# Kernel tuning notes

Measured on AMD Instinct MI355X. Metric: run time of the kernel, lower is better.

## Reference

```python
import jax, jax.numpy as jnp
import numpy as np

B, V, K, D, E, NE = 32, 512, 16, 128, 32, 8192


def setup_inputs() -> dict:
    key = jax.random.key(0)
    ks = jax.random.split(key, 12)
    s = 0.05
    return {
        "vertex_features": jax.random.normal(ks[0], (B, V, D), jnp.float32),
        "atom_adj": jax.random.randint(ks[1], (B * V * K,), 0, B * V),
        "bond_adj": jax.random.randint(ks[2], (B * V * K,), 0, B * NE),
        "h0": jax.random.normal(ks[3], (B, V, D), jnp.float32),
        "lamda": jnp.full((1,), 0.5, jnp.float32),
        "alpha": jnp.full((1,), 0.1, jnp.float32),
        "l": 1,
        "edge_initial": jax.random.normal(ks[4], (B, NE, E), jnp.float32),
        "vertex_mask": jnp.ones((B, V), jnp.float32),
        "nbs_mask": jax.random.uniform(ks[5], (B, V, K), jnp.float32),
        # label_U1: (D+E) -> D ; label_U2: 2D -> D ; feature_updating: D -> D (variant=False)
        "W1": jax.random.normal(ks[6], (D, D + E), jnp.float32) * s,
        "b1": jax.random.normal(ks[7], (D,), jnp.float32) * s,
        "W2": jax.random.normal(ks[8], (D, 2 * D), jnp.float32) * s,
        "b2": jax.random.normal(ks[9], (D,), jnp.float32) * s,
        "W3": jax.random.normal(ks[10], (D, D), jnp.float32) * s,
        "b3": jax.random.normal(ks[11], (D,), jnp.float32) * s,
    }


def reference(vertex_features, atom_adj, bond_adj, h0, lamda, alpha, l,
              edge_initial, vertex_mask, nbs_mask, W1, b1, W2, b2, W3, b3):
    b, v = vertex_mask.shape
    k = nbs_mask.shape[2]
    d = vertex_features.shape[-1]
    e = edge_initial.shape[-1]
    # gather neighbor vertex and edge features (flat index, torch.index_select semantics)
    vn = vertex_features.reshape(-1, d)[atom_adj].reshape(b, v, k, d)
    en = edge_initial.reshape(-1, e)[bond_adj].reshape(b, v, k, e)
    l_neighbor = jnp.concatenate([vn, en], axis=-1)            # [b,v,k,d+e]
    nl = jax.nn.gelu(l_neighbor @ W1.T + b1, approximate=False)  # exact GELU like torch F.gelu
    nl = jnp.sum(nl * nbs_mask[..., None], axis=-2)            # masked sum over neighbors -> [b,v,d]
    hi = jnp.concatenate([nl, vertex_features], axis=-1) @ W2.T + b2
    theta = jnp.log(lamda / l + 1.0)                           # broadcast scalar (shape [1])
    support = (1.0 - alpha) * hi + alpha * h0                  # variant=False: r == support
    out = theta * (support @ W3.T + b3) + (1.0 - theta) * support
    out = out + vertex_features                                # residual=True
    return out
```

## Files before the change

### kernel.cpp

```cpp
#include <hip/hip_runtime.h>
#include <hip/hip_bf16.h>
#include <math.h>

#define NLSTR 136

typedef __bf16 bf16x8 __attribute__((ext_vector_type(8)));
typedef float f32x4 __attribute__((ext_vector_type(4)));
typedef float f32x16 __attribute__((ext_vector_type(16)));
typedef unsigned short ushort8v __attribute__((ext_vector_type(8)));

union FragU { ushort8v u; bf16x8 b; };

static __device__ inline unsigned short f2bf(float f){
  unsigned u = __float_as_uint(f);
  u += 0x7fffu + ((u >> 16) & 1u);
  return (unsigned short)(u >> 16);
}
static __device__ inline float bf2f(unsigned short u){
  return __uint_as_float(((unsigned)u) << 16);
}

static __device__ inline float gelu_f(float x){
  float u = x * x;
  float p = fmaf(u, 0.07135481283f, 1.5957691216f);
  float t = x * p;
  float e = __builtin_amdgcn_exp2f(t * -1.44269504f);
  return x * __builtin_amdgcn_rcpf(1.0f + e);
}

__global__ __launch_bounds__(256) void prep_kernel(
    const float* __restrict__ vf, const float* __restrict__ W1,
    const float* __restrict__ W2, const float* __restrict__ W3,
    unsigned short* __restrict__ vfbf, unsigned short* __restrict__ w1f,
    unsigned short* __restrict__ w2f, unsigned short* __restrict__ w3f)
{
  int t = blockIdx.x * 256 + threadIdx.x;
  if (t < 262144){
    const float4* src = (const float4*)vf;
    float4 x = src[t * 2], y = src[t * 2 + 1];
    ushort8v o;
    o[0]=f2bf(x.x); o[1]=f2bf(x.y); o[2]=f2bf(x.z); o[3]=f2bf(x.w);
    o[4]=f2bf(y.x); o[5]=f2bf(y.y); o[6]=f2bf(y.z); o[7]=f2bf(y.w);
    *(ushort8v*)(vfbf + t * 8) = o;
    return;
  }
  int t2 = t - 262144;
  const float* s;
  unsigned short* d;
  if (t2 < 2560){
    int fragid = t2 >> 6, lane = t2 & 63;
    int kc = fragid >> 2, nc2 = fragid & 3, n = lane & 31, h = lane >> 5;
    s = W1 + (nc2 * 32 + n) * 160 + kc * 16 + h * 8;
    d = w1f + t2 * 8;
  } else if (t2 < 6656){
    int t3 = t2 - 2560;
    int fragid = t3 >> 6, lane = t3 & 63;
    int kc = fragid >> 3, nc = fragid & 7, col = lane & 15, quad = lane >> 4;
    s = W2 + (nc * 16 + col) * 256 + kc * 32 + quad * 8;
    d = w2f + t3 * 8;
  } else if (t2 < 8704){
    int t3 = t2 - 6656;
    int fragid = t3 >> 6, lane = t3 & 63;
    int kc = fragid >> 3, nc = fragid & 7, col = lane & 15, quad = lane >> 4;
    s = W3 + (nc * 16 + col) * 128 + kc * 32 + quad * 8;
    d = w3f + t3 * 8;
  } else return;
#pragma unroll
  for (int j = 0; j < 8; j++) d[j] = f2bf(s[j]);
}

__global__ __launch_bounds__(256) void fused_kernel(
    const unsigned short* __restrict__ vfbf,
    const int* __restrict__ aadj, const int* __restrict__ badj,
    const float* __restrict__ edge, const float* __restrict__ nbs,
    const float* __restrict__ h0,
    const unsigned short* __restrict__ w1f, const unsigned short* __restrict__ w2f,
    const unsigned short* __restrict__ w3f,
    const float* __restrict__ b1, const float* __restrict__ b2, const float* __restrict__ b3,
    const float* __restrict__ lamda, const float* __restrict__ alpha,
    const int* __restrict__ lval,
    float* __restrict__ out)
{
  __shared__ __align__(16) unsigned short nl_lds[16 * NLSTR];
  __shared__ __align__(16) unsigned short sup_lds[16 * NLSTR];
  const int wid  = threadIdx.x >> 6;
  const int lane = threadIdx.x & 63;
  const int n32  = lane & 31;
  const int h    = lane >> 5;
  const int nb   = lane & 15;
  const int vsel = (lane >> 4) & 1;
  const int col  = lane & 15;
  const int quad = lane >> 4;
  const int v0   = blockIdx.x * 16;

  float b1v[4];
#pragma unroll
  for (int nc2 = 0; nc2 < 4; nc2++) b1v[nc2] = b1[nc2 * 32 + n32];

  const ushort8v* w1v = (const ushort8v*)w1f;
  const float4*   nbs4 = (const float4*)nbs;

  for (int itp = 0; itp < 2; ++itp){
    const int vA  = v0 + wid * 4 + itp * 2;
    const int vtx = vA + vsel;
    const int a = aadj[vtx * 16 + nb];
    const int e = badj[vtx * 16 + nb];

    ushort8v av[8];
    const ushort8v* arow = (const ushort8v*)(vfbf + (size_t)a * 128 + h * 8);
#pragma unroll
    for (int kc = 0; kc < 8; kc++) av[kc] = arow[kc * 2];
    float4 e0a = *(const float4*)(edge + (size_t)e * 32 + h * 8);
    float4 e0b = *(const float4*)(edge + (size_t)e * 32 + h * 8 + 4);
    float4 e1a = *(const float4*)(edge + (size_t)e * 32 + 16 + h * 8);
    float4 e1b = *(const float4*)(edge + (size_t)e * 32 + 16 + h * 8 + 4);
    const float4 mAlo = nbs4[vA * 4 + h],       mAhi = nbs4[vA * 4 + 2 + h];
    const float4 mBlo = nbs4[(vA + 1) * 4 + h], mBhi = nbs4[(vA + 1) * 4 + 2 + h];

    FragU ef[2];
    ef[0].u[0]=f2bf(e0a.x); ef[0].u[1]=f2bf(e0a.y); ef[0].u[2]=f2bf(e0a.z); ef[0].u[3]=f2bf(e0a.w);
    ef[0].u[4]=f2bf(e0b.x); ef[0].u[5]=f2bf(e0b.y); ef[0].u[6]=f2bf(e0b.z); ef[0].u[7]=f2bf(e0b.w);
    ef[1].u[0]=f2bf(e1a.x); ef[1].u[1]=f2bf(e1a.y); ef[1].u[2]=f2bf(e1a.z); ef[1].u[3]=f2bf(e1a.w);
    ef[1].u[4]=f2bf(e1b.x); ef[1].u[5]=f2bf(e1b.y); ef[1].u[6]=f2bf(e1b.z); ef[1].u[7]=f2bf(e1b.w);

    f32x16 acc[4] = {};
#pragma unroll
    for (int kc = 0; kc < 10; kc++){
      FragU fa;
      if (kc < 8) fa.u = av[kc];
      else        fa.u = ef[kc - 8].u;
#pragma unroll
      for (int nc2 = 0; nc2 < 4; nc2++){
        FragU bf_;
        bf_.u = w1v[(kc * 4 + nc2) * 64 + lane];
        acc[nc2] = __builtin_amdgcn_mfma_f32_32x32x16_bf16(fa.b, bf_.b, acc[nc2], 0, 0, 0);
      }
    }

    const int row = wid * 4 + itp * 2;
#pragma unroll
    for (int nc2 = 0; nc2 < 4; nc2++){
      const float bb = b1v[nc2];
      f32x16 ac = acc[nc2];
      float sA = gelu_f(ac[0] + bb) * mAlo.x + gelu_f(ac[1] + bb) * mAlo.y
               + gelu_f(ac[2] + bb) * mAlo.z + gelu_f(ac[3] + bb) * mAlo.w
               + gelu_f(ac[4] + bb) * mAhi.x + gelu_f(ac[5] + bb) * mAhi.y
               + gelu_f(ac[6] + bb) * mAhi.z + gelu_f(ac[7] + bb) * mAhi.w;
      float sB = gelu_f(ac[8] + bb) * mBlo.x + gelu_f(ac[9] + bb) * mBlo.y
               + gelu_f(ac[10] + bb) * mBlo.z + gelu_f(ac[11] + bb) * mBlo.w
               + gelu_f(ac[12] + bb) * mBhi.x + gelu_f(ac[13] + bb) * mBhi.y
               + gelu_f(ac[14] + bb) * mBhi.z + gelu_f(ac[15] + bb) * mBhi.w;
      sA += __shfl_xor(sA, 32, 64);
      sB += __shfl_xor(sB, 32, 64);
      if (h == 0) nl_lds[row * NLSTR + nc2 * 32 + n32] = f2bf(sA);
      else        nl_lds[(row + 1) * NLSTR + nc2 * 32 + n32] = f2bf(sB);
    }
  }
  __syncthreads();

  const int nc0 = 2 * wid;
  const float th = logf(lamda[0] / (float)lval[0] + 1.0f);
  const float al = alpha[0];

  f32x4 acc2[2] = {};
#pragma unroll
  for (int kc = 0; kc < 8; kc++){
    FragU a;
    if (kc < 4) a.u = *(const ushort8v*)(nl_lds + col * NLSTR + kc * 32 + quad * 8);
    else        a.u = *(const ushort8v*)(vfbf + (size_t)(v0 + col) * 128 + (kc - 4) * 32 + quad * 8);
#pragma unroll
    for (int p = 0; p < 2; p++){
      FragU bf_;
      bf_.u = *(const ushort8v*)(w2f + ((kc * 8 + nc0 + p) * 64 + lane) * 8);
      acc2[p] = __builtin_amdgcn_mfma_f32_16x16x32_bf16(a.b, bf_.b, acc2[p], 0, 0, 0);
    }
  }

  float sup[2][4];
#pragma unroll
  for (int p = 0; p < 2; p++){
    const int d = (nc0 + p) * 16 + col;
    const float bb = b2[d];
#pragma unroll
    for (int r = 0; r < 4; r++){
      const int vtx = v0 + quad * 4 + r;
      float hi = acc2[p][r] + bb;
      float s = (1.f - al) * hi + al * h0[vtx * 128 + d];
      sup[p][r] = s;
      sup_lds[(quad * 4 + r) * NLSTR + d] = f2bf(s);
    }
  }
  __syncthreads();

  f32x4 acc3[2] = {};
#pragma unroll
  for (int kc = 0; kc < 4; kc++){
    FragU a;
    a.u = *(const ushort8v*)(sup_lds + col * NLSTR + kc * 32 + quad * 8);
#pragma unroll
    for (int p = 0; p < 2; p++){
      FragU bf_;
      bf_.u = *(const ushort8v*)(w3f + ((kc * 8 + nc0 + p) * 64 + lane) * 8);
      acc3[p] = __builtin_amdgcn_mfma_f32_16x16x32_bf16(a.b, bf_.b, acc3[p], 0, 0, 0);
    }
  }

#pragma unroll
  for (int p = 0; p < 2; p++){
    const int d = (nc0 + p) * 16 + col;
    const float bb = b3[d];
#pragma unroll
    for (int r = 0; r < 4; r++){
      const int vtx = v0 + quad * 4 + r;
      float res = bf2f(vfbf[(size_t)vtx * 128 + d]);
      out[vtx * 128 + d] = th * (acc3[p][r] + bb) + (1.f - th) * sup[p][r] + res;
    }
  }
}

extern "C" void kernel_launch(void* const* d_in, const int* in_sizes, int n_in,
                              void* d_out, int out_size, void* d_ws, size_t ws_size,
                              hipStream_t stream)
{
  const float* vfp  = (const float*)d_in[0];
  const int*   aadj = (const int*)d_in[1];
  const int*   badj = (const int*)d_in[2];
  const float* h0   = (const float*)d_in[3];
  const float* lam  = (const float*)d_in[4];
  const float* alp  = (const float*)d_in[5];
  const int*   lv   = (const int*)d_in[6];
  const float* edge = (const float*)d_in[7];
  const float* nbs  = (const float*)d_in[9];
  const float* W1   = (const float*)d_in[10];
  const float* b1   = (const float*)d_in[11];
  const float* W2   = (const float*)d_in[12];
  const float* b2   = (const float*)d_in[13];
  const float* W3   = (const float*)d_in[14];
  const float* b3   = (const float*)d_in[15];
  float* out = (float*)d_out;

  unsigned short* w1f  = (unsigned short*)d_ws;
  unsigned short* w2f  = w1f + 20480;
  unsigned short* w3f  = w2f + 32768;
  unsigned short* vfbf = w3f + 16384;

  prep_kernel<<<1058, 256, 0, stream>>>(vfp, W1, W2, W3, vfbf, w1f, w2f, w3f);
  fused_kernel<<<1024, 256, 0, stream>>>(vfbf, aadj, badj, edge, nbs, h0,
                                         w1f, w2f, w3f, b1, b2, b3, lam, alp, lv, out);
}
```

Measured before the change: 149.8 us.

## Stage W1 in LDS, software-pipeline neighbor gathers, use packed bf16 converts

Each block now copies the pre-swizzled W1 fragments (40KB) into shared memory and reads the MFMA B operands from LDS instead of global memory. The two-iteration neighbor loop is unrolled by hand so the second gather (vertex rows, edge features, masks) is issued before the first iteration's GELU/mask reduction, overlapping gather latency with compute. Scalar fp32-to-bf16 rounding is replaced with the packed float2-to-bfloat162 conversion. The extra 40KB of LDS per block and the higher register pressure may reduce occupancy.

```diff
diff --git a/kernel.cpp b/kernel.cpp
--- a/kernel.cpp
+++ b/kernel.cpp
@@ -18,6 +18,17 @@
 }
 static __device__ inline float bf2f(unsigned short u){
   return __uint_as_float(((unsigned)u) << 16);
+}
+static __device__ inline unsigned pk2(float a, float b){
+  union { __hip_bfloat162 h; unsigned u; } r;
+  r.h = __float22bfloat162_rn(float2{a, b});
+  return r.u;
+}
+static __device__ inline ushort8v pkcvt8(float4 a, float4 b){
+  union { unsigned u[4]; ushort8v v; } r;
+  r.u[0] = pk2(a.x, a.y); r.u[1] = pk2(a.z, a.w);
+  r.u[2] = pk2(b.x, b.y); r.u[3] = pk2(b.z, b.w);
+  return r.v;
 }
 
 static __device__ inline float gelu_f(float x){
@@ -38,10 +49,7 @@
   if (t < 262144){
     const float4* src = (const float4*)vf;
     float4 x = src[t * 2], y = src[t * 2 + 1];
-    ushort8v o;
-    o[0]=f2bf(x.x); o[1]=f2bf(x.y); o[2]=f2bf(x.z); o[3]=f2bf(x.w);
-    o[4]=f2bf(y.x); o[5]=f2bf(y.y); o[6]=f2bf(y.z); o[7]=f2bf(y.w);
-    *(ushort8v*)(vfbf + t * 8) = o;
+    *(ushort8v*)(vfbf + t * 8) = pkcvt8(x, y);
     return;
   }
   int t2 = t - 262144;
@@ -81,6 +89,7 @@
     const int* __restrict__ lval,
     float* __restrict__ out)
 {
+  __shared__ __align__(16) ushort8v w1s[2560];
   __shared__ __align__(16) unsigned short nl_lds[16 * NLSTR];
   __shared__ __align__(16) unsigned short sup_lds[16 * NLSTR];
   const int wid  = threadIdx.x >> 6;
@@ -93,63 +102,133 @@
   const int quad = lane >> 4;
   const int v0   = blockIdx.x * 16;
 
+  {
+    const ushort8v* src = (const ushort8v*)w1f;
+#pragma unroll
+    for (int i = 0; i < 10; i++)
+      w1s[threadIdx.x + 256 * i] = src[threadIdx.x + 256 * i];
+  }
+
   float b1v[4];
 #pragma unroll
   for (int nc2 = 0; nc2 < 4; nc2++) b1v[nc2] = b1[nc2 * 32 + n32];
 
-  const ushort8v* w1v = (const ushort8v*)w1f;
-  const float4*   nbs4 = (const float4*)nbs;
-
-  for (int itp = 0; itp < 2; ++itp){
-    const int vA  = v0 + wid * 4 + itp * 2;
-    const int vtx = vA + vsel;
-    const int a = aadj[vtx * 16 + nb];
-    const int e = badj[vtx * 16 + nb];
-
-    ushort8v av[8];
-    const ushort8v* arow = (const ushort8v*)(vfbf + (size_t)a * 128 + h * 8);
-#pragma unroll
-    for (int kc = 0; kc < 8; kc++) av[kc] = arow[kc * 2];
-    float4 e0a = *(const float4*)(edge + (size_t)e * 32 + h * 8);
-    float4 e0b = *(const float4*)(edge + (size_t)e * 32 + h * 8 + 4);
-    float4 e1a = *(const float4*)(edge + (size_t)e * 32 + 16 + h * 8);
-    float4 e1b = *(const float4*)(edge + (size_t)e * 32 + 16 + h * 8 + 4);
-    const float4 mAlo = nbs4[vA * 4 + h],       mAhi = nbs4[vA * 4 + 2 + h];
-    const float4 mBlo = nbs4[(vA + 1) * 4 + h], mBhi = nbs4[(vA + 1) * 4 + 2 + h];
-
-    FragU ef[2];
-    ef[0].u[0]=f2bf(e0a.x); ef[0].u[1]=f2bf(e0a.y); ef[0].u[2]=f2bf(e0a.z); ef[0].u[3]=f2bf(e0a.w);
-    ef[0].u[4]=f2bf(e0b.x); ef[0].u[5]=f2bf(e0b.y); ef[0].u[6]=f2bf(e0b.z); ef[0].u[7]=f2bf(e0b.w);
-    ef[1].u[0]=f2bf(e1a.x); ef[1].u[1]=f2bf(e1a.y); ef[1].u[2]=f2bf(e1a.z); ef[1].u[3]=f2bf(e1a.w);
-    ef[1].u[4]=f2bf(e1b.x); ef[1].u[5]=f2bf(e1b.y); ef[1].u[6]=f2bf(e1b.z); ef[1].u[7]=f2bf(e1b.w);
-
-    f32x16 acc[4] = {};
-#pragma unroll
-    for (int kc = 0; kc < 10; kc++){
-      FragU fa;
-      if (kc < 8) fa.u = av[kc];
-      else        fa.u = ef[kc - 8].u;
-#pragma unroll
-      for (int nc2 = 0; nc2 < 4; nc2++){
-        FragU bf_;
-        bf_.u = w1v[(kc * 4 + nc2) * 64 + lane];
-        acc[nc2] = __builtin_amdgcn_mfma_f32_32x32x16_bf16(fa.b, bf_.b, acc[nc2], 0, 0, 0);
-      }
-    }
-
-    const int row = wid * 4 + itp * 2;
+  const float4* nbs4 = (const float4*)nbs;
+  const int vA0 = v0 + wid * 4;
+
+  const int a0 = aadj[(vA0 + vsel) * 16 + nb];
+  const int e0 = badj[(vA0 + vsel) * 16 + nb];
+  ushort8v av0[8];
+  {
+    const ushort8v* arow = (const ushort8v*)(vfbf + (size_t)a0 * 128 + h * 8);
+#pragma unroll
+    for (int kc = 0; kc < 8; kc++) av0[kc] = arow[kc * 2];
+  }
+  float4 e0a = *(const float4*)(edge + (size_t)e0 * 32 + h * 8);
+  float4 e0b = *(const float4*)(edge + (size_t)e0 * 32 + h * 8 + 4);
+  float4 e0c = *(const float4*)(edge + (size_t)e0 * 32 + 16 + h * 8);
+  float4 e0d = *(const float4*)(edge + (size_t)e0 * 32 + 16 + h * 8 + 4);
+  const float4 m0Alo = nbs4[vA0 * 4 + h],       m0Ahi = nbs4[vA0 * 4 + 2 + h];
+  const float4 m0Blo = nbs4[(vA0 + 1) * 4 + h], m0Bhi = nbs4[(vA0 + 1) * 4 + 2 + h];
+
+  __syncthreads();
+
+  FragU ef0[2];
+  ef0[0].u = pkcvt8(e0a, e0b);
+  ef0[1].u = pkcvt8(e0c, e0d);
+
+  f32x16 acc[4] = {};
+#pragma unroll
+  for (int kc = 0; kc < 8; kc++){
+    FragU fa; fa.u = av0[kc];
+#pragma unroll
+    for (int nc2 = 0; nc2 < 4; nc2++){
+      FragU bf_; bf_.u = w1s[(kc * 4 + nc2) * 64 + lane];
+      acc[nc2] = __builtin_amdgcn_mfma_f32_32x32x16_bf16(fa.b, bf_.b, acc[nc2], 0, 0, 0);
+    }
+  }
+#pragma unroll
+  for (int kc = 8; kc < 10; kc++){
+    FragU fa; fa.u = ef0[kc - 8].u;
+#pragma unroll
+    for (int nc2 = 0; nc2 < 4; nc2++){
+      FragU bf_; bf_.u = w1s[(kc * 4 + nc2) * 64 + lane];
+      acc[nc2] = __builtin_amdgcn_mfma_f32_32x32x16_bf16(fa.b, bf_.b, acc[nc2], 0, 0, 0);
+    }
+  }
+
+  const int a1 = aadj[(vA0 + 2 + vsel) * 16 + nb];
+  const int e1 = badj[(vA0 + 2 + vsel) * 16 + nb];
+  ushort8v av1[8];
+  {
+    const ushort8v* arow = (const ushort8v*)(vfbf + (size_t)a1 * 128 + h * 8);
+#pragma unroll
+    for (int kc = 0; kc < 8; kc++) av1[kc] = arow[kc * 2];
+  }
+  float4 e1a = *(const float4*)(edge + (size_t)e1 * 32 + h * 8);
+  float4 e1b = *(const float4*)(edge + (size_t)e1 * 32 + h * 8 + 4);
+  float4 e1c = *(const float4*)(edge + (size_t)e1 * 32 + 16 + h * 8);
+  float4 e1d = *(const float4*)(edge + (size_t)e1 * 32 + 16 + h * 8 + 4);
+  const float4 m1Alo = nbs4[(vA0 + 2) * 4 + h], m1Ahi = nbs4[(vA0 + 2) * 4 + 2 + h];
+  const float4 m1Blo = nbs4[(vA0 + 3) * 4 + h], m1Bhi = nbs4[(vA0 + 3) * 4 + 2 + h];
+
+  {
+    const int row = wid * 4;
 #pragma unroll
     for (int nc2 = 0; nc2 < 4; nc2++){
       const float bb = b1v[nc2];
       f32x16 ac = acc[nc2];
-      float sA = gelu_f(ac[0] + bb) * mAlo.x + gelu_f(ac[1] + bb) * mAlo.y
-               + gelu_f(ac[2] + bb) * mAlo.z + gelu_f(ac[3] + bb) * mAlo.w
-               + gelu_f(ac[4] + bb) * mAhi.x + gelu_f(ac[5] + bb) * mAhi.y
-               + gelu_f(ac[6] + bb) * mAhi.z + gelu_f(ac[7] + bb) * mAhi.w;
-      float sB = gelu_f(ac[8] + bb) * mBlo.x + gelu_f(ac[9] + bb) * mBlo.y
-               + gelu_f(ac[10] + bb) * mBlo.z + gelu_f(ac[11] + bb) * mBlo.w
-               + gelu_f(ac[12] + bb) * mBhi.x + gelu_f(ac[13] + bb) * mBhi.y
-               + gelu_f(ac[14] + bb) * mBhi.z + gelu_f(ac[15] + bb) * mBhi.w;
+      float sA = gelu_f(ac[0] + bb) * m0Alo.x + gelu_f(ac[1] + bb) * m0Alo.y
+               + gelu_f(ac[2] + bb) * m0Alo.z + gelu_f(ac[3] + bb) * m0Alo.w
+               + gelu_f(ac[4] + bb) * m0Ahi.x + gelu_f(ac[5] + bb) * m0Ahi.y
+               + gelu_f(ac[6] + bb) * m0Ahi.z + gelu_f(ac[7] + bb) * m0Ahi.w;
+      float sB = gelu_f(ac[8] + bb) * m0Blo.x + gelu_f(ac[9] + bb) * m0Blo.y
+               + gelu_f(ac[10] + bb) * m0Blo.z + gelu_f(ac[11] + bb) * m0Blo.w
+               + gelu_f(ac[12] + bb) * m0Bhi.x + gelu_f(ac[13] + bb) * m0Bhi.y
+               + gelu_f(ac[14] + bb) * m0Bhi.z + gelu_f(ac[15] + bb) * m0Bhi.w;
+      sA += __shfl_xor(sA, 32, 64);
+      sB += __shfl_xor(sB, 32, 64);
+      if (h == 0) nl_lds[row * NLSTR + nc2 * 32 + n32] = f2bf(sA);
+      else        nl_lds[(row + 1) * NLSTR + nc2 * 32 + n32] = f2bf(sB);
+    }
+  }
+
+  {
+    FragU ef1[2];
+    ef1[0].u = pkcvt8(e1a, e1b);
+    ef1[1].u = pkcvt8(e1c, e1d);
+    f32x16 acc1[4] = {};
+#pragma unroll
+    for (int kc = 0; kc < 8; kc++){
+      FragU fa; fa.u = av1[kc];
+#pragma unroll
+      for (int nc2 = 0; nc2 < 4; nc2++){
+        FragU bf_; bf_.u = w1s[(kc * 4 + nc2) * 64 + lane];
+        acc1[nc2] = __builtin_amdgcn_mfma_f32_32x32x16_bf16(fa.b, bf_.b, acc1[nc2], 0, 0, 0);
+      }
+    }
+#pragma unroll
+    for (int kc = 8; kc < 10; kc++){
+      FragU fa; fa.u = ef1[kc - 8].u;
+#pragma unroll
+      for (int nc2 = 0; nc2 < 4; nc2++){
+        FragU bf_; bf_.u = w1s[(kc * 4 + nc2) * 64 + lane];
+        acc1[nc2] = __builtin_amdgcn_mfma_f32_32x32x16_bf16(fa.b, bf_.b, acc1[nc2], 0, 0, 0);
+      }
+    }
+    const int row = wid * 4 + 2;
+#pragma unroll
+    for (int nc2 = 0; nc2 < 4; nc2++){
+      const float bb = b1v[nc2];
+      f32x16 ac = acc1[nc2];
+      float sA = gelu_f(ac[0] + bb) * m1Alo.x + gelu_f(ac[1] + bb) * m1Alo.y
+               + gelu_f(ac[2] + bb) * m1Alo.z + gelu_f(ac[3] + bb) * m1Alo.w
+               + gelu_f(ac[4] + bb) * m1Ahi.x + gelu_f(ac[5] + bb) * m1Ahi.y
+               + gelu_f(ac[6] + bb) * m1Ahi.z + gelu_f(ac[7] + bb) * m1Ahi.w;
+      float sB = gelu_f(ac[8] + bb) * m1Blo.x + gelu_f(ac[9] + bb) * m1Blo.y
+               + gelu_f(ac[10] + bb) * m1Blo.z + gelu_f(ac[11] + bb) * m1Blo.w
+               + gelu_f(ac[12] + bb) * m1Bhi.x + gelu_f(ac[13] + bb) * m1Bhi.y
+               + gelu_f(ac[14] + bb) * m1Bhi.z + gelu_f(ac[15] + bb) * m1Bhi.w;
       sA += __shfl_xor(sA, 32, 64);
       sB += __shfl_xor(sB, 32, 64);
       if (h == 0) nl_lds[row * NLSTR + nc2 * 32 + n32] = f2bf(sA);
```

Measured after the change: 156.8 us. 4.7% more time.

## Stage gathered neighbor rows in double-buffered LDS and keep W1 slice in registers

Applied to the files above, without the earlier changes.

Each wave now owns one 32-column slice of W1, loaded once into registers, instead of streaming all W1 fragments from global memory for every vertex pair. Gathered neighbor vertex and edge rows are loaded cooperatively by the whole block into double-buffered shared memory and prefetched one step ahead, overlapping the gather with MFMA work. The W1 fragment layout in the prep kernel is reordered to match, and float-to-bf16 conversion uses packed intrinsics. This adds a barrier per step and extra LDS use, which may reduce occupancy.

```diff
diff --git a/kernel.cpp b/kernel.cpp
--- a/kernel.cpp
+++ b/kernel.cpp
@@ -3,6 +3,7 @@
 #include <math.h>
 
 #define NLSTR 136
+#define ASTR  168
 
 typedef __bf16 bf16x8 __attribute__((ext_vector_type(8)));
 typedef float f32x4 __attribute__((ext_vector_type(4)));
@@ -18,6 +19,17 @@
 }
 static __device__ inline float bf2f(unsigned short u){
   return __uint_as_float(((unsigned)u) << 16);
+}
+static __device__ inline unsigned pk2(float a, float b){
+  union { __hip_bfloat162 h; unsigned u; } r;
+  r.h = __float22bfloat162_rn(float2{a, b});
+  return r.u;
+}
+static __device__ inline ushort8v pkcvt8(float4 a, float4 b){
+  union { unsigned u[4]; ushort8v v; } r;
+  r.u[0] = pk2(a.x, a.y); r.u[1] = pk2(a.z, a.w);
+  r.u[2] = pk2(b.x, b.y); r.u[3] = pk2(b.z, b.w);
+  return r.v;
 }
 
 static __device__ inline float gelu_f(float x){
@@ -38,10 +50,7 @@
   if (t < 262144){
     const float4* src = (const float4*)vf;
     float4 x = src[t * 2], y = src[t * 2 + 1];
-    ushort8v o;
-    o[0]=f2bf(x.x); o[1]=f2bf(x.y); o[2]=f2bf(x.z); o[3]=f2bf(x.w);
-    o[4]=f2bf(y.x); o[5]=f2bf(y.y); o[6]=f2bf(y.z); o[7]=f2bf(y.w);
-    *(ushort8v*)(vfbf + t * 8) = o;
+    *(ushort8v*)(vfbf + t * 8) = pkcvt8(x, y);
     return;
   }
   int t2 = t - 262144;
@@ -49,7 +58,7 @@
   unsigned short* d;
   if (t2 < 2560){
     int fragid = t2 >> 6, lane = t2 & 63;
-    int kc = fragid >> 2, nc2 = fragid & 3, n = lane & 31, h = lane >> 5;
+    int nc2 = fragid / 10, kc = fragid % 10, n = lane & 31, h = lane >> 5;
     s = W1 + (nc2 * 32 + n) * 160 + kc * 16 + h * 8;
     d = w1f + t2 * 8;
   } else if (t2 < 6656){
@@ -81,79 +90,86 @@
     const int* __restrict__ lval,
     float* __restrict__ out)
 {
+  __shared__ __align__(16) unsigned short abuf[2][32 * ASTR];
   __shared__ __align__(16) unsigned short nl_lds[16 * NLSTR];
   __shared__ __align__(16) unsigned short sup_lds[16 * NLSTR];
   const int wid  = threadIdx.x >> 6;
   const int lane = threadIdx.x & 63;
   const int n32  = lane & 31;
   const int h    = lane >> 5;
-  const int nb   = lane & 15;
-  const int vsel = (lane >> 4) & 1;
   const int col  = lane & 15;
   const int quad = lane >> 4;
   const int v0   = blockIdx.x * 16;
 
-  float b1v[4];
-#pragma unroll
-  for (int nc2 = 0; nc2 < 4; nc2++) b1v[nc2] = b1[nc2 * 32 + n32];
-
-  const ushort8v* w1v = (const ushort8v*)w1f;
-  const float4*   nbs4 = (const float4*)nbs;
-
-  for (int itp = 0; itp < 2; ++itp){
-    const int vA  = v0 + wid * 4 + itp * 2;
-    const int vtx = vA + vsel;
-    const int a = aadj[vtx * 16 + nb];
-    const int e = badj[vtx * 16 + nb];
-
-    ushort8v av[8];
-    const ushort8v* arow = (const ushort8v*)(vfbf + (size_t)a * 128 + h * 8);
-#pragma unroll
-    for (int kc = 0; kc < 8; kc++) av[kc] = arow[kc * 2];
-    float4 e0a = *(const float4*)(edge + (size_t)e * 32 + h * 8);
-    float4 e0b = *(const float4*)(edge + (size_t)e * 32 + h * 8 + 4);
-    float4 e1a = *(const float4*)(edge + (size_t)e * 32 + 16 + h * 8);
-    float4 e1b = *(const float4*)(edge + (size_t)e * 32 + 16 + h * 8 + 4);
-    const float4 mAlo = nbs4[vA * 4 + h],       mAhi = nbs4[vA * 4 + 2 + h];
-    const float4 mBlo = nbs4[(vA + 1) * 4 + h], mBhi = nbs4[(vA + 1) * 4 + 2 + h];
-
-    FragU ef[2];
-    ef[0].u[0]=f2bf(e0a.x); ef[0].u[1]=f2bf(e0a.y); ef[0].u[2]=f2bf(e0a.z); ef[0].u[3]=f2bf(e0a.w);
-    ef[0].u[4]=f2bf(e0b.x); ef[0].u[5]=f2bf(e0b.y); ef[0].u[6]=f2bf(e0b.z); ef[0].u[7]=f2bf(e0b.w);
-    ef[1].u[0]=f2bf(e1a.x); ef[1].u[1]=f2bf(e1a.y); ef[1].u[2]=f2bf(e1a.z); ef[1].u[3]=f2bf(e1a.w);
-    ef[1].u[4]=f2bf(e1b.x); ef[1].u[5]=f2bf(e1b.y); ef[1].u[6]=f2bf(e1b.z); ef[1].u[7]=f2bf(e1b.w);
-
-    f32x16 acc[4] = {};
+  FragU bw[10];
+#pragma unroll
+  for (int kc = 0; kc < 10; kc++)
+    bw[kc].u = *(const ushort8v*)(w1f + ((wid * 10 + kc) * 64 + lane) * 8);
+
+  const float bb1 = b1[wid * 32 + n32];
+  const float4* nbs4 = (const float4*)nbs;
+
+  const int srow = threadIdx.x >> 3;
+  const int ssub = threadIdx.x & 7;
+
+  ushort8v sv0, sv1; float4 se;
+  {
+    const int vtx = v0 + (srow >> 4), nb = srow & 15;
+    const int a = aadj[vtx * 16 + nb], e = badj[vtx * 16 + nb];
+    const ushort8v* vs = (const ushort8v*)(vfbf + (size_t)a * 128 + ssub * 16);
+    sv0 = vs[0]; sv1 = vs[1];
+    se = *(const float4*)(edge + (size_t)e * 32 + ssub * 4);
+  }
+  {
+    unsigned short* dst = abuf[0] + srow * ASTR + ssub * 16;
+    *(ushort8v*)dst = sv0; *(ushort8v*)(dst + 8) = sv1;
+    unsigned* ed = (unsigned*)(abuf[0] + srow * ASTR + 128 + ssub * 4);
+    ed[0] = pk2(se.x, se.y); ed[1] = pk2(se.z, se.w);
+  }
+
+#pragma unroll 1
+  for (int p = 0; p < 8; ++p){
+    __syncthreads();
+    if (p < 7){
+      const int vtx = v0 + 2 * (p + 1) + (srow >> 4), nb = srow & 15;
+      const int a = aadj[vtx * 16 + nb], e = badj[vtx * 16 + nb];
+      const ushort8v* vs = (const ushort8v*)(vfbf + (size_t)a * 128 + ssub * 16);
+      sv0 = vs[0]; sv1 = vs[1];
+      se = *(const float4*)(edge + (size_t)e * 32 + ssub * 4);
+    }
+
+    const unsigned short* ab = abuf[p & 1] + n32 * ASTR + h * 8;
+    f32x16 acc = {};
 #pragma unroll
     for (int kc = 0; kc < 10; kc++){
       FragU fa;
-      if (kc < 8) fa.u = av[kc];
-      else        fa.u = ef[kc - 8].u;
-#pragma unroll
-      for (int nc2 = 0; nc2 < 4; nc2++){
-        FragU bf_;
-        bf_.u = w1v[(kc * 4 + nc2) * 64 + lane];
-        acc[nc2] = __builtin_amdgcn_mfma_f32_32x32x16_bf16(fa.b, bf_.b, acc[nc2], 0, 0, 0);
-      }
-    }
-
-    const int row = wid * 4 + itp * 2;
-#pragma unroll
-    for (int nc2 = 0; nc2 < 4; nc2++){
-      const float bb = b1v[nc2];
-      f32x16 ac = acc[nc2];
-      float sA = gelu_f(ac[0] + bb) * mAlo.x + gelu_f(ac[1] + bb) * mAlo.y
-               + gelu_f(ac[2] + bb) * mAlo.z + gelu_f(ac[3] + bb) * mAlo.w
-               + gelu_f(ac[4] + bb) * mAhi.x + gelu_f(ac[5] + bb) * mAhi.y
-               + gelu_f(ac[6] + bb) * mAhi.z + gelu_f(ac[7] + bb) * mAhi.w;
-      float sB = gelu_f(ac[8] + bb) * mBlo.x + gelu_f(ac[9] + bb) * mBlo.y
-               + gelu_f(ac[10] + bb) * mBlo.z + gelu_f(ac[11] + bb) * mBlo.w
-               + gelu_f(ac[12] + bb) * mBhi.x + gelu_f(ac[13] + bb) * mBhi.y
-               + gelu_f(ac[14] + bb) * mBhi.z + gelu_f(ac[15] + bb) * mBhi.w;
+      fa.u = *(const ushort8v*)(ab + kc * 16);
+      acc = __builtin_amdgcn_mfma_f32_32x32x16_bf16(fa.b, bw[kc].b, acc, 0, 0, 0);
+    }
+
+    {
+      const int vA = v0 + 2 * p;
+      const float4 mAlo = nbs4[vA * 4 + h],       mAhi = nbs4[vA * 4 + 2 + h];
+      const float4 mBlo = nbs4[(vA + 1) * 4 + h], mBhi = nbs4[(vA + 1) * 4 + 2 + h];
+      float sA = gelu_f(acc[0] + bb1) * mAlo.x + gelu_f(acc[1] + bb1) * mAlo.y
+               + gelu_f(acc[2] + bb1) * mAlo.z + gelu_f(acc[3] + bb1) * mAlo.w
+               + gelu_f(acc[4] + bb1) * mAhi.x + gelu_f(acc[5] + bb1) * mAhi.y
+               + gelu_f(acc[6] + bb1) * mAhi.z + gelu_f(acc[7] + bb1) * mAhi.w;
+      float sB = gelu_f(acc[8] + bb1) * mBlo.x + gelu_f(acc[9] + bb1) * mBlo.y
+               + gelu_f(acc[10] + bb1) * mBlo.z + gelu_f(acc[11] + bb1) * mBlo.w
+               + gelu_f(acc[12] + bb1) * mBhi.x + gelu_f(acc[13] + bb1) * mBhi.y
+               + gelu_f(acc[14] + bb1) * mBhi.z + gelu_f(acc[15] + bb1) * mBhi.w;
       sA += __shfl_xor(sA, 32, 64);
       sB += __shfl_xor(sB, 32, 64);
-      if (h == 0) nl_lds[row * NLSTR + nc2 * 32 + n32] = f2bf(sA);
-      else        nl_lds[(row + 1) * NLSTR + nc2 * 32 + n32] = f2bf(sB);
+      if (h == 0) nl_lds[(2 * p)     * NLSTR + wid * 32 + n32] = f2bf(sA);
+      else        nl_lds[(2 * p + 1) * NLSTR + wid * 32 + n32] = f2bf(sB);
+    }
+
+    if (p < 7){
+      unsigned short* dst = abuf[(p + 1) & 1] + srow * ASTR + ssub * 16;
+      *(ushort8v*)dst = sv0; *(ushort8v*)(dst + 8) = sv1;
+      unsigned* ed = (unsigned*)(abuf[(p + 1) & 1] + srow * ASTR + 128 + ssub * 4);
+      ed[0] = pk2(se.x, se.y); ed[1] = pk2(se.z, se.w);
     }
   }
   __syncthreads();
@@ -169,24 +185,24 @@
     if (kc < 4) a.u = *(const ushort8v*)(nl_lds + col * NLSTR + kc * 32 + quad * 8);
     else        a.u = *(const ushort8v*)(vfbf + (size_t)(v0 + col) * 128 + (kc - 4) * 32 + quad * 8);
 #pragma unroll
-    for (int p = 0; p < 2; p++){
+    for (int pq = 0; pq < 2; pq++){
       FragU bf_;
-      bf_.u = *(const ushort8v*)(w2f + ((kc * 8 + nc0 + p) * 64 + lane) * 8);
-      acc2[p] = __builtin_amdgcn_mfma_f32_16x16x32_bf16(a.b, bf_.b, acc2[p], 0, 0, 0);
+      bf_.u = *(const ushort8v*)(w2f + ((kc * 8 + nc0 + pq) * 64 + lane) * 8);
+      acc2[pq] = __builtin_amdgcn_mfma_f32_16x16x32_bf16(a.b, bf_.b, acc2[pq], 0, 0, 0);
     }
   }
 
   float sup[2][4];
 #pragma unroll
-  for (int p = 0; p < 2; p++){
-    const int d = (nc0 + p) * 16 + col;
+  for (int pq = 0; pq < 2; pq++){
+    const int d = (nc0 + pq) * 16 + col;
     const float bb = b2[d];
 #pragma unroll
     for (int r = 0; r < 4; r++){
       const int vtx = v0 + quad * 4 + r;
-      float hi = acc2[p][r] + bb;
+      float hi = acc2[pq][r] + bb;
       float s = (1.f - al) * hi + al * h0[vtx * 128 + d];
-      sup[p][r] = s;
+      sup[pq][r] = s;
       sup_lds[(quad * 4 + r) * NLSTR + d] = f2bf(s);
     }
   }
@@ -198,22 +214,22 @@
     FragU a;
     a.u = *(const ushort8v*)(sup_lds + col * NLSTR + kc * 32 + quad * 8);
 #pragma unroll
-    for (int p = 0; p < 2; p++){
+    for (int pq = 0; pq < 2; pq++){
       FragU bf_;
-      bf_.u = *(const ushort8v*)(w3f + ((kc * 8 + nc0 + p) * 64 + lane) * 8);
-      acc3[p] = __builtin_amdgcn_mfma_f32_16x16x32_bf16(a.b, bf_.b, acc3[p], 0, 0, 0);
-    }
-  }
-
-#pragma unroll
-  for (int p = 0; p < 2; p++){
-    const int d = (nc0 + p) * 16 + col;
+      bf_.u = *(const ushort8v*)(w3f + ((kc * 8 + nc0 + pq) * 64 + lane) * 8);
+      acc3[pq] = __builtin_amdgcn_mfma_f32_16x16x32_bf16(a.b, bf_.b, acc3[pq], 0, 0, 0);
+    }
+  }
+
+#pragma unroll
+  for (int pq = 0; pq < 2; pq++){
+    const int d = (nc0 + pq) * 16 + col;
     const float bb = b3[d];
 #pragma unroll
     for (int r = 0; r < 4; r++){
       const int vtx = v0 + quad * 4 + r;
       float res = bf2f(vfbf[(size_t)vtx * 128 + d]);
-      out[vtx * 128 + d] = th * (acc3[p][r] + bb) + (1.f - th) * sup[p][r] + res;
+      out[vtx * 128 + d] = th * (acc3[pq][r] + bb) + (1.f - th) * sup[pq][r] + res;
     }
   }
 }
```

Result: no change. 147.3 us (-1.7%).
